# Optimization experiments

Hardware: AMD Instinct MI355X
Metric: run time of the kernel (lower is better)

Reference implementation:

```python
import jax, jax.numpy as jnp
import numpy as np

B, D, N_CLASSES = 8192, 256, 64
MARGIN = 0.5


def setup_inputs() -> dict:
    key = jax.random.key(0)
    k1, k2 = jax.random.split(key)
    emb = jax.random.normal(k1, (B, D), dtype=jnp.float32)
    emb = emb / jnp.linalg.norm(emb, axis=1, keepdims=True)  # module expects L2-normalised
    labels = jax.random.randint(k2, (B,), 0, N_CLASSES)
    return {"embeddings": emb, "labels": labels}


def _pairwise_dist(x):
    # torch.cdist(x, x, p=2): sqrt of clamped squared distances, safe at 0 for grads
    sq = jnp.sum(x * x, axis=1)
    d2 = jnp.maximum(sq[:, None] + sq[None, :] - 2.0 * (x @ x.T), 0.0)
    safe = jnp.where(d2 > 0.0, d2, 1.0)
    return jnp.where(d2 > 0.0, jnp.sqrt(safe), 0.0)


def reference(embeddings, labels):
    # Vectorized semi-hard mining: for each anchor,
    #   d_ap = max positive distance; the mined negative is the MIN negative
    #   distance (argmin over the semi-hard subset == global neg argmin when
    #   that min is < d_ap + margin; otherwise the subset is empty -> skip).
    dist = _pairwise_dist(embeddings)            # [B, B]
    n = labels.shape[0]
    same = labels[:, None] == labels[None, :]
    eye = jnp.eye(n, dtype=bool)
    pos_mask = same & ~eye
    neg_mask = ~same

    NEG = jnp.float32(-1e30)
    POS = jnp.float32(1e30)
    d_ap = jnp.max(jnp.where(pos_mask, dist, NEG), axis=1)   # hardest positive
    d_an = jnp.min(jnp.where(neg_mask, dist, POS), axis=1)   # closest negative

    has_pos = jnp.any(pos_mask, axis=1)
    has_neg = jnp.any(neg_mask, axis=1)
    valid = has_pos & has_neg & (d_an < d_ap + MARGIN)       # semi-hard exists

    losses = jax.nn.relu(d_ap - d_an + MARGIN)
    count = jnp.sum(valid)
    total = jnp.sum(jnp.where(valid, losses, 0.0))
    zero = jnp.sum(embeddings) * 0.0
    return jnp.where(count > 0, total / jnp.maximum(count, 1).astype(losses.dtype), zero)
```

## Files before the change

### kernel.cpp

```cpp
#include <hip/hip_runtime.h>
#include <hip/hip_bf16.h>

#define Bn 8192
#define Dn 256
#define MARGIN_F 0.5f

typedef short short8 __attribute__((ext_vector_type(8)));
typedef float floatx4 __attribute__((ext_vector_type(4)));

__device__ inline unsigned short f2bf(float f) {
    unsigned int u = __float_as_uint(f);
    unsigned int r = (u + 0x7fffu + ((u >> 16) & 1u)) >> 16;
    return (unsigned short)r;
}

#define OFF_SQ   ((size_t)Bn * Dn * 2)
#define OFF_POS  (OFF_SQ + Bn * 4)
#define OFF_NEG  (OFF_POS + Bn * 4)
#define OFF_ACC  (OFF_NEG + Bn * 4)

__global__ __launch_bounds__(256) void prep_kernel(
        const float* __restrict__ emb, unsigned short* __restrict__ embT,
        float* __restrict__ sq, unsigned int* __restrict__ posb,
        unsigned int* __restrict__ negb, unsigned int* __restrict__ accs) {
    const int w = threadIdx.x >> 6;
    const int lane = threadIdx.x & 63;
    const int row = blockIdx.x * 4 + w;

    const float4 v = *(const float4*)(emb + (size_t)row * Dn + lane * 4);
    float ss = v.x * v.x + v.y * v.y + v.z * v.z + v.w * v.w;
    #pragma unroll
    for (int m = 32; m >= 1; m >>= 1) ss += __shfl_xor(ss, m);

    uint2 o;
    o.x = (unsigned int)f2bf(v.x) | ((unsigned int)f2bf(v.y) << 16);
    o.y = (unsigned int)f2bf(v.z) | ((unsigned int)f2bf(v.w) << 16);
    const int kg = lane >> 1;
    *(uint2*)(embT + ((size_t)kg * Bn + row) * 8 + (lane & 1) * 4) = o;

    if (lane == 0) {
        sq[row] = ss;
        posb[row] = 0u;
        negb[row] = 0xFFFFFFFFu;
    }
    if (blockIdx.x == 0 && threadIdx.x == 0) {
        accs[0] = 0u; accs[1] = 0u; accs[2] = 0u;
    }
}

__global__ __launch_bounds__(256, 2) void mine_kernel(
        const unsigned short* __restrict__ embT, const float* __restrict__ sq,
        const int* __restrict__ labels, unsigned int* __restrict__ posb,
        unsigned int* __restrict__ negb) {
    const int tid  = threadIdx.x;
    const int w    = tid >> 6;
    const int lane = tid & 63;
    const int quad = lane >> 4;
    const int c    = lane & 15;

    const int iBase = blockIdx.x * 256 + w * 64;
    const int jBase = blockIdx.y * 256;

    const size_t KS = (size_t)4 * Bn * 8;

    __shared__ __align__(16) unsigned short Bt[2][32 * 32 * 8];
    __shared__ float sqJ[256];
    __shared__ int   labJ[256];

    short8 aFrag[4][8];
    #pragma unroll
    for (int m = 0; m < 4; ++m) {
        const unsigned short* ap = embT + ((size_t)quad * Bn + iBase + m * 16 + c) * 8;
        #pragma unroll
        for (int ks = 0; ks < 8; ++ks)
            aFrag[m][ks] = *(const short8*)(ap + ks * KS);
    }
    #pragma unroll
    for (int m = 0; m < 4; ++m)
        #pragma unroll
        for (int ks = 0; ks < 8; ++ks)
            asm volatile("" : "+v"(aFrag[m][ks]));

    int labI[4][4];
    #pragma unroll
    for (int m = 0; m < 4; ++m)
        #pragma unroll
        for (int r = 0; r < 4; ++r)
            labI[m][r] = labels[iBase + m * 16 + quad * 4 + r];

    float rpos[4][4], rneg[4][4];
    #pragma unroll
    for (int m = 0; m < 4; ++m)
        #pragma unroll
        for (int r = 0; r < 4; ++r) { rpos[m][r] = -1e30f; rneg[m][r] = 1e30f; }

    sqJ[tid]  = sq[jBase + tid];
    labJ[tid] = labels[jBase + tid];

    const unsigned short* sbase = embT + ((size_t)(tid >> 5) * Bn + jBase + (tid & 31)) * 8;

    #define STAGE(BUF, JT) do {                                                        \
        const unsigned short* _s = sbase + (size_t)(JT) * 32 * 8;                      \
        unsigned short* _d = &Bt[BUF][(size_t)tid * 8];                                \
        _Pragma("unroll")                                                              \
        for (int cc = 0; cc < 4; ++cc)                                                 \
            __builtin_amdgcn_global_load_lds(                                          \
                (const __attribute__((address_space(1))) unsigned int*)                \
                    (_s + (size_t)cc * 8 * Bn * 8),                                    \
                (__attribute__((address_space(3))) unsigned int*)(_d + cc * 256 * 8),  \
                16, 0, 0);                                                             \
    } while (0)

    STAGE(0, 0);
    __syncthreads();

    for (int jt = 0; jt < 8; ++jt) {
        if (jt + 1 < 8) STAGE((jt + 1) & 1, jt + 1);
        const unsigned short* bt = Bt[jt & 1];
        #pragma unroll
        for (int n = 0; n < 2; ++n) {
            const int jc = jt * 32 + n * 16 + c;
            const float sj = sqJ[jc];
            const int   lj = labJ[jc];
            floatx4 acc[4];
            #pragma unroll
            for (int m = 0; m < 4; ++m) acc[m] = (floatx4){0.f, 0.f, 0.f, 0.f};
            #pragma unroll
            for (int ks = 0; ks < 8; ++ks) {
                short8 bF = *(const short8*)(bt +
                    (size_t)((ks * 4 + quad) * 32 + n * 16 + c) * 8);
                #pragma unroll
                for (int m = 0; m < 4; ++m)
                    acc[m] = __builtin_amdgcn_mfma_f32_16x16x32_bf16(
                        aFrag[m][ks], bF, acc[m], 0, 0, 0);
            }
            #pragma unroll
            for (int m = 0; m < 4; ++m)
                #pragma unroll
                for (int r = 0; r < 4; ++r) {
                    float s = fmaf(-2.0f, acc[m][r], sj);
                    bool  e = (lj == labI[m][r]);
                    rpos[m][r] = e ? fmaxf(rpos[m][r], s) : rpos[m][r];
                    rneg[m][r] = e ? rneg[m][r] : fminf(rneg[m][r], s);
                }
        }
        __syncthreads();
    }
    #undef STAGE

    #pragma unroll
    for (int m = 0; m < 4; ++m)
        #pragma unroll
        for (int r = 0; r < 4; ++r) {
            float p = rpos[m][r], q = rneg[m][r];
            #pragma unroll
            for (int msk = 1; msk <= 8; msk <<= 1) {
                p = fmaxf(p, __shfl_xor(p, msk));
                q = fminf(q, __shfl_xor(q, msk));
            }
            if (c == 0) {
                int ig = iBase + m * 16 + quad * 4 + r;
                if (p > -1e29f) atomicMax(&posb[ig], __float_as_uint(p + 4.0f));
                if (q <  1e29f) atomicMin(&negb[ig], __float_as_uint(q + 4.0f));
            }
        }
}

__global__ __launch_bounds__(256) void finalize_kernel(
        const float* __restrict__ sq, const unsigned int* __restrict__ posb,
        const unsigned int* __restrict__ negb, float* __restrict__ accsF,
        unsigned int* __restrict__ accsU, float* __restrict__ out) {
    const int i = blockIdx.x * 256 + threadIdx.x;
    unsigned int pb = posb[i], nb = negb[i];
    bool hp = (pb != 0u);
    bool hn = (nb != 0xFFFFFFFFu);
    float si  = sq[i];
    float dap = sqrtf(fmaxf(si + (__uint_as_float(pb) - 4.0f), 0.0f));
    float dan = sqrtf(fmaxf(si + (__uint_as_float(nb) - 4.0f), 0.0f));
    bool valid = hp && hn && (dan < dap + MARGIN_F);
    float t  = valid ? fmaxf(dap - dan + MARGIN_F, 0.0f) : 0.0f;
    float cc = valid ? 1.0f : 0.0f;
    #pragma unroll
    for (int m = 32; m >= 1; m >>= 1) {
        t  += __shfl_xor(t, m);
        cc += __shfl_xor(cc, m);
    }
    __shared__ float sT[4], sC[4];
    int w = threadIdx.x >> 6, lane = threadIdx.x & 63;
    if (lane == 0) { sT[w] = t; sC[w] = cc; }
    __syncthreads();
    if (threadIdx.x == 0) {
        atomicAdd(&accsF[0], sT[0] + sT[1] + sT[2] + sT[3]);
        atomicAdd(&accsF[1], sC[0] + sC[1] + sC[2] + sC[3]);
        __threadfence();
        unsigned int ticket = atomicAdd(&accsU[2], 1u);
        if (ticket == gridDim.x - 1) {
            float tot = atomicAdd(&accsF[0], 0.0f);
            float cnt = atomicAdd(&accsF[1], 0.0f);
            out[0] = (cnt > 0.0f) ? tot / cnt : 0.0f;
        }
    }
}

extern "C" void kernel_launch(void* const* d_in, const int* in_sizes, int n_in,
                              void* d_out, int out_size, void* d_ws, size_t ws_size,
                              hipStream_t stream) {
    const float* emb   = (const float*)d_in[0];
    const int*  labels = (const int*)d_in[1];
    float* out = (float*)d_out;

    char* ws = (char*)d_ws;
    unsigned short* embT = (unsigned short*)ws;
    float*        sqv  = (float*)(ws + OFF_SQ);
    unsigned int* posb = (unsigned int*)(ws + OFF_POS);
    unsigned int* negb = (unsigned int*)(ws + OFF_NEG);
    float*        accsF = (float*)(ws + OFF_ACC);
    unsigned int* accsU = (unsigned int*)(ws + OFF_ACC);

    prep_kernel<<<Bn / 4, 256, 0, stream>>>(emb, embT, sqv, posb, negb, accsU);
    mine_kernel<<<dim3(32, 32), 256, 0, stream>>>(embT, sqv, labels, posb, negb);
    finalize_kernel<<<Bn / 256, 256, 0, stream>>>(sqv, posb, negb, accsF, accsU, out);
}
```

Before: 111.0 us.

## Exploit distance matrix symmetry by computing only upper-triangular block tiles

The mining grid shrinks from all 32x32 block tiles to the 528 upper-triangular tiles. Each off-diagonal tile also reduces its Gram results column-wise and pushes them into the column rows' positive and negative extrema with atomics. This roughly halves the MFMA work and the tile loads. In exchange it adds extra VALU work, cross-lane shuffles and many more global atomics inside the inner loop, and the block count per wave of CUs is uneven.

```diff
diff --git a/kernel.cpp b/kernel.cpp
--- a/kernel.cpp
+++ b/kernel.cpp
@@ -58,8 +58,13 @@
     const int quad = lane >> 4;
     const int c    = lane & 15;
 
-    const int iBase = blockIdx.x * 256 + w * 64;
-    const int jBase = blockIdx.y * 256;
+    int bi = 0, rem = blockIdx.x, rowlen = 32;
+    while (rem >= rowlen) { rem -= rowlen; --rowlen; ++bi; }
+    const int bj = bi + rem;
+    const bool offdiag = (bi != bj);
+
+    const int iBase = bi * 256 + w * 64;
+    const int jBase = bj * 256;
 
     const size_t KS = (size_t)4 * Bn * 8;
 
@@ -81,12 +86,16 @@
         for (int ks = 0; ks < 8; ++ks)
             asm volatile("" : "+v"(aFrag[m][ks]));
 
-    int labI[4][4];
-    #pragma unroll
-    for (int m = 0; m < 4; ++m)
-        #pragma unroll
-        for (int r = 0; r < 4; ++r)
-            labI[m][r] = labels[iBase + m * 16 + quad * 4 + r];
+    int   labI[4][4];
+    float sqI[4][4];
+    #pragma unroll
+    for (int m = 0; m < 4; ++m)
+        #pragma unroll
+        for (int r = 0; r < 4; ++r) {
+            const int ig = iBase + m * 16 + quad * 4 + r;
+            labI[m][r] = labels[ig];
+            sqI[m][r]  = sq[ig];
+        }
 
     float rpos[4][4], rneg[4][4];
     #pragma unroll
@@ -134,15 +143,33 @@
                     acc[m] = __builtin_amdgcn_mfma_f32_16x16x32_bf16(
                         aFrag[m][ks], bF, acc[m], 0, 0, 0);
             }
+            float jp = -1e30f, jq = 1e30f;
             #pragma unroll
             for (int m = 0; m < 4; ++m)
                 #pragma unroll
                 for (int r = 0; r < 4; ++r) {
-                    float s = fmaf(-2.0f, acc[m][r], sj);
-                    bool  e = (lj == labI[m][r]);
+                    const float d = acc[m][r];
+                    const bool  e = (lj == labI[m][r]);
+                    float s = fmaf(-2.0f, d, sj);
                     rpos[m][r] = e ? fmaxf(rpos[m][r], s) : rpos[m][r];
                     rneg[m][r] = e ? rneg[m][r] : fminf(rneg[m][r], s);
+                    if (offdiag) {
+                        float s2 = fmaf(-2.0f, d, sqI[m][r]);
+                        jp = e ? fmaxf(jp, s2) : jp;
+                        jq = e ? jq : fminf(jq, s2);
+                    }
                 }
+            if (offdiag) {
+                jp = fmaxf(jp, __shfl_xor(jp, 16));
+                jp = fmaxf(jp, __shfl_xor(jp, 32));
+                jq = fminf(jq, __shfl_xor(jq, 16));
+                jq = fminf(jq, __shfl_xor(jq, 32));
+                if (quad == 0) {
+                    const int jg = jBase + jt * 32 + n * 16 + c;
+                    if (jp > -1e29f) atomicMax(&posb[jg], __float_as_uint(jp + 4.0f));
+                    if (jq <  1e29f) atomicMin(&negb[jg], __float_as_uint(jq + 4.0f));
+                }
+            }
         }
         __syncthreads();
     }
@@ -218,6 +245,6 @@
     unsigned int* accsU = (unsigned int*)(ws + OFF_ACC);
 
     prep_kernel<<<Bn / 4, 256, 0, stream>>>(emb, embT, sqv, posb, negb, accsU);
-    mine_kernel<<<dim3(32, 32), 256, 0, stream>>>(embT, sqv, labels, posb, negb);
+    mine_kernel<<<528, 256, 0, stream>>>(embT, sqv, labels, posb, negb);
     finalize_kernel<<<Bn / 256, 256, 0, stream>>>(sqv, posb, negb, accsF, accsU, out);
 }
```

Result: slower. 122.6 us (+10.4%).
